# Kernel optimization log

Hardware: AMD Instinct MI355X
Metric: run time of the kernel (lower is better)

The kernel has to match this reference:

```python
import jax, jax.numpy as jnp
import numpy as np

B, N = 4, 512
C_IN, H, W = 1024, 48, 48
IMG_H, IMG_W = 48.0, 48.0
CNN_EMB, BOX_EMB, GCN_OUT = 512, 256, 512
ROWS, COLS = 58, 30
ALPHA = 5.0
K_EDGES = 8 * N  # edges kept per image per graph

# all directed pairs (i != j) of a fully-connected graph on N nodes
_ii, _jj = np.meshgrid(np.arange(N), np.arange(N), indexing='ij')
_m = _ii != _jj
PAIRS = jnp.asarray(np.stack([_ii[_m], _jj[_m]], axis=1).astype(np.int32))  # [E,2]


def setup_inputs():
    key = jax.random.key(0)
    ks = jax.random.split(key, 12)
    x = jax.random.normal(ks[0], (B, C_IN, H, W), jnp.float32)
    # valid boxes (x1<x2, y1<y2) inside the 48x48 feature map
    p = jax.random.uniform(ks[1], (B, N, 2, 2), minval=0.0, maxval=float(W) - 2.0)
    lo = jnp.min(p, axis=2)
    hi = jnp.max(p, axis=2) + 1.0
    boxes = jnp.concatenate([lo, hi], axis=-1)  # [B,N,4] x1,y1,x2,y2

    def lin(k, fi, fo):
        return jax.random.normal(k, (fi, fo), jnp.float32) / np.sqrt(fi)

    return {
        'input': x, 'boxes': boxes,
        'im_scales': jnp.ones((B,), jnp.float32),
        'pdls': jnp.zeros((B,), jnp.float32),
        'pdts': jnp.zeros((B,), jnp.float32),
        'W_dec': jax.random.normal(ks[2], (256, C_IN, 3, 3), jnp.float32) / np.sqrt(C_IN * 9.0),
        'b_dec': jnp.zeros((256,), jnp.float32),
        'W_box': lin(ks[3], 4, BOX_EMB), 'b_box': jnp.zeros((BOX_EMB,), jnp.float32),
        'W_cnn': lin(ks[4], 256 * 4, CNN_EMB), 'b_cnn': jnp.zeros((CNN_EMB,), jnp.float32),
        'W_grow': lin(ks[5], CNN_EMB + BOX_EMB, GCN_OUT), 'b_grow': jnp.zeros((GCN_OUT,), jnp.float32),
        'W_gcol': lin(ks[6], CNN_EMB + BOX_EMB, GCN_OUT), 'b_gcol': jnp.zeros((GCN_OUT,), jnp.float32),
        'W_rcls': lin(ks[7], GCN_OUT, 2 * (ROWS - 1) * 2), 'b_rcls': jnp.zeros((2 * (ROWS - 1) * 2,), jnp.float32),
        'W_ccls': lin(ks[8], GCN_OUT, 2 * (COLS - 1) * 2), 'b_ccls': jnp.zeros((2 * (COLS - 1) * 2,), jnp.float32),
    }


def _bilinear(feat, bidx, py, px):
    # feat [B,C,H,W]; py,px [M,4] sample coords -> [M,4,C]
    Hh, Ww = feat.shape[2], feat.shape[3]
    py = jnp.clip(py, 0.0, Hh - 1.0)
    px = jnp.clip(px, 0.0, Ww - 1.0)
    y0 = jnp.floor(py).astype(jnp.int32)
    x0 = jnp.floor(px).astype(jnp.int32)
    y1 = jnp.minimum(y0 + 1, Hh - 1)
    x1 = jnp.minimum(x0 + 1, Ww - 1)
    wy = (py - y0)[..., None]
    wx = (px - x0)[..., None]
    b = bidx[:, None]
    f00 = feat[b, :, y0, x0]
    f01 = feat[b, :, y0, x1]
    f10 = feat[b, :, y1, x0]
    f11 = feat[b, :, y1, x1]
    return f00 * (1 - wy) * (1 - wx) + f01 * (1 - wy) * wx + f10 * wy * (1 - wx) + f11 * wy * wx


def _roi_align_2x2(feat, boxes, bidx):
    # roi_align output_size=2, spatial_scale=1, one sample per bin (bin center)
    x1, y1, x2, y2 = boxes[:, 0], boxes[:, 1], boxes[:, 2], boxes[:, 3]
    bw = (x2 - x1) / 2.0
    bh = (y2 - y1) / 2.0
    offs = jnp.array([0.5, 1.5], jnp.float32)
    sx = x1[:, None] + offs * bw[:, None]  # [M,2]
    sy = y1[:, None] + offs * bh[:, None]
    py = sy[:, jnp.array([0, 0, 1, 1])]  # (iy, ix) ordering
    px = sx[:, jnp.array([0, 1, 0, 1])]
    val = _bilinear(feat, bidx, py, px)  # [M,4,C]
    return jnp.transpose(val, (0, 2, 1)).reshape(val.shape[0], -1)  # [M, C*2*2]


def _edge_attrs(boxes_i, scale, pdl, pdt):
    org = (boxes_i - jnp.stack([pdl, pdt, pdl, pdt])) / scale
    cx = (org[:, 0] + org[:, 2]) * 0.5
    cy = (org[:, 1] + org[:, 3]) * 0.5
    tb_w = jnp.max(org[:, jnp.array([0, 2])])
    tb_h = jnp.max(org[:, jnp.array([1, 3])])
    s, d = PAIRS[:, 0], PAIRS[:, 1]
    row_attr = jnp.exp(-jnp.square((cy[s] - cy[d]) * ALPHA / tb_h))
    col_attr = jnp.exp(-jnp.square((cx[s] - cx[d]) * ALPHA / tb_w))
    rv, ri = jax.lax.top_k(row_attr, K_EDGES)
    cv, ci = jax.lax.top_k(col_attr, K_EDGES)
    return rv, PAIRS[ri], cv, PAIRS[ci]


def _gcn(x, Wg, bg, edges, ew, num_nodes):
    # PyG GCNConv: self-loops with weight 1, symmetric normalization
    loop = jnp.arange(num_nodes, dtype=edges.dtype)
    src = jnp.concatenate([edges[0], loop])
    dst = jnp.concatenate([edges[1], loop])
    w = jnp.concatenate([ew, jnp.ones((num_nodes,), ew.dtype)])
    deg = jax.ops.segment_sum(w, dst, num_segments=num_nodes)
    dis = jax.lax.rsqrt(deg)  # deg >= 1 thanks to self-loops
    norm = dis[src] * w * dis[dst]
    xw = x @ Wg
    agg = jax.ops.segment_sum(norm[:, None] * xw[src], dst, num_segments=num_nodes)
    return agg + bg


def _forward(input, boxes, im_scales, pdls, pdts, W_dec, b_dec, W_box, b_box,
             W_cnn, b_cnn, W_grow, b_grow, W_gcol, b_gcol, W_rcls, b_rcls, W_ccls, b_ccls):
    Bn = B * N
    flat = boxes.reshape(Bn, 4)
    # box features (relative center / size)
    cx = (flat[:, 0] + flat[:, 2]) / 2.0
    cy = (flat[:, 1] + flat[:, 3]) / 2.0
    bf = jnp.stack([cx / IMG_W, cy / IMG_H,
                    (flat[:, 2] - flat[:, 0]) / IMG_W,
                    (flat[:, 3] - flat[:, 1]) / IMG_H], axis=1)
    box_feat = jax.nn.relu(bf @ W_box + b_box)
    # decode conv + relu
    dec = jax.lax.conv_general_dilated(input, W_dec, (1, 1), 'SAME',
                                       dimension_numbers=('NCHW', 'OIHW', 'NCHW'))
    dec = jax.nn.relu(dec + b_dec[None, :, None, None])
    # roi-align 2x2 + cnn embedding
    bidx = jnp.repeat(jnp.arange(B, dtype=jnp.int32), N)
    cnn = _roi_align_2x2(dec, flat, bidx)
    cnn_feat = jax.nn.relu(cnn @ W_cnn + b_cnn)
    # per-image dense graph -> top-8N row/col edges
    rv, re, cv, ce = jax.vmap(_edge_attrs)(boxes, im_scales, pdls, pdts)
    off = (jnp.arange(B, dtype=jnp.int32) * N)[:, None, None]
    row_edge = (re + off).reshape(-1, 2).T  # [2, B*K]
    col_edge = (ce + off).reshape(-1, 2).T
    row_w = rv.reshape(-1)
    col_w = cv.reshape(-1)
    fusion = jnp.concatenate([box_feat, cnn_feat], axis=1)  # [Bn, 768]
    row_feat = jax.nn.relu(_gcn(fusion, W_grow, b_grow, row_edge, row_w, Bn))
    col_feat = jax.nn.relu(_gcn(fusion, W_gcol, b_gcol, col_edge, col_w, Bn))
    row_score = jax.nn.leaky_relu(row_feat @ W_rcls + b_rcls, 0.01).reshape(Bn, 2, ROWS - 1, 2)
    col_score = jax.nn.leaky_relu(col_feat @ W_ccls + b_ccls, 0.01).reshape(Bn, 2, COLS - 1, 2)
    return row_score, col_score


def reference(input, boxes, im_scales, pdls, pdts, W_dec, b_dec, W_box, b_box,
              W_cnn, b_cnn, W_grow, b_grow, W_gcol, b_gcol, W_rcls, b_rcls, W_ccls, b_ccls):
    return _forward(input, boxes, im_scales, pdls, pdts, W_dec, b_dec, W_box, b_box,
                    W_cnn, b_cnn, W_grow, b_grow, W_gcol, b_gcol,
                    W_rcls, b_rcls, W_ccls, b_ccls)
```

## Files before the change

kernel.cpp:

```cpp
#include <hip/hip_runtime.h>
#include <cstdint>
#include <math.h>

typedef unsigned int u32;
typedef unsigned long long u64;
typedef unsigned short ushort;

typedef __attribute__((ext_vector_type(8))) _Float16 f16x8;
typedef __attribute__((ext_vector_type(4))) _Float16 f16x4;
typedef __attribute__((ext_vector_type(4))) float f32x4;

#define NB    4
#define BnN   2048
#define NE    261632
#define NCHUNK 16
#define ECHUNK 16352
#define KEDGE 4096
#define TIECAP 2048
#define PSLICE 2359296
#define MS    64
#define TS    64

__global__ __launch_bounds__(256) void cvt_x_kernel(
    const float* __restrict__ in, _Float16* __restrict__ xf)
{
    __shared__ _Float16 sh[64][49];
    int cg = blockIdx.x, y = blockIdx.y, b = blockIdx.z;
    int tid = threadIdx.x;
    for (int i = tid; i < 64 * 48; i += 256) {
        int cl = i / 48, x = i - cl * 48;
        sh[cl][x] = (_Float16)in[(((size_t)b * 1024 + cg * 64 + cl) * 48 + y) * 48 + x];
    }
    __syncthreads();
    for (int i = tid; i < 64 * 48; i += 256) {
        int x = i / 64, cl = i - x * 64;
        xf[((size_t)(b * 48 + y) * 48 + x) * 1024 + cg * 64 + cl] = sh[cl][x];
    }
}

__global__ __launch_bounds__(256) void cvt_w_kernel(
    const float* __restrict__ W, _Float16* __restrict__ wf)
{
    __shared__ _Float16 sh[9216];
    int o = blockIdx.x, tid = threadIdx.x;
    for (int g = tid; g < 9216; g += 256)
        sh[g] = (_Float16)W[(size_t)o * 9216 + g];
    __syncthreads();
    for (int g = tid; g < 9216; g += 256) {
        int tap = g >> 10, ch = g & 1023;
        wf[(size_t)o * 9216 + g] = sh[ch * 9 + tap];
    }
}

__global__ __launch_bounds__(256) void cvt_t5_kernel(
    const float* __restrict__ Wc,  _Float16* __restrict__ WcT,
    const float* __restrict__ Wgr, _Float16* __restrict__ WgrT,
    const float* __restrict__ Wgc, _Float16* __restrict__ WgcT,
    const float* __restrict__ Wr,  _Float16* __restrict__ WrT,
    const float* __restrict__ Wcc, _Float16* __restrict__ WccT)
{
    __shared__ _Float16 sh[32][33];
    int bid = blockIdx.x;
    const float* in; _Float16* out; int K, N, tx0, ty0, ntx;
    if (bid < 512)       { in = Wc;  out = WcT;  K = 1024; N = 512; ntx = 16; bid -= 0;    }
    else if (bid < 896)  { in = Wgr; out = WgrT; K = 768;  N = 512; ntx = 16; bid -= 512;  }
    else if (bid < 1280) { in = Wgc; out = WgcT; K = 768;  N = 512; ntx = 16; bid -= 896;  }
    else if (bid < 1408) { in = Wr;  out = WrT;  K = 512;  N = 228; ntx = 8;  bid -= 1280; }
    else                 { in = Wcc; out = WccT; K = 512;  N = 116; ntx = 4;  bid -= 1408; }
    tx0 = (bid % ntx) * 32;
    ty0 = (bid / ntx) * 32;
    int tx = threadIdx.x & 31, ty = threadIdx.x >> 5;
#pragma unroll
    for (int i = 0; i < 4; ++i) {
        int k = ty0 + ty + i * 8, n = tx0 + tx;
        sh[ty + i * 8][tx] = (k < K && n < N) ? (_Float16)in[(size_t)k * N + n] : (_Float16)0.f;
    }
    __syncthreads();
#pragma unroll
    for (int i = 0; i < 4; ++i) {
        int n = tx0 + ty + i * 8, k = ty0 + tx;
        if (n < N && k < K) out[(size_t)n * K + k] = sh[tx][ty + i * 8];
    }
}

#define GLD16(gsrc, ldst)                                                    \
    __builtin_amdgcn_global_load_lds(                                        \
        (const __attribute__((address_space(1))) void*)(gsrc),               \
        (__attribute__((address_space(3))) void*)(ldst), 16, 0, 0)

#define STAGE(cc)                                                            \
    {                                                                        \
        _Pragma("unroll")                                                    \
        for (int it = 0; it < 5; ++it) {                                     \
            if (it * 256 + wv * 64 < 1152)                                   \
                GLD16(wsrc[it] + (cc), &wS[(it * 256 + wv * 64) * 8]);       \
        }                                                                    \
        _Pragma("unroll")                                                    \
        for (int it = 0; it < 8; ++it)                                       \
            GLD16(xsrc[it] + (cc), &xS[(it * 256 + wv * 64) * 8]);           \
    }

__global__ __launch_bounds__(256) void conv_part_kernel(
    const _Float16* __restrict__ xf, const _Float16* __restrict__ wf,
    const _Float16* __restrict__ zbuf, float* __restrict__ pbuf)
{
    __shared__ _Float16 wS[1152 * 8];
    __shared__ _Float16 xS[2048 * 8];
    const int p = blockIdx.x;
    const int L = (p & 7) * 96 + (p >> 3);
    const int og = L & 7;
    const int t  = L >> 3;
    const int xt = t % 6;
    const int bz = t / 6;
    const int y0 = xt * 8;
    const int b  = bz >> 2, ks = bz & 3;
    const int tid = threadIdx.x;
    const int wv = tid >> 6;
    const int ln = tid & 63;
    const int n  = ln & 15;
    const int q  = ln >> 4;

    f32x4 acc[2][2][3];
#pragma unroll
    for (int mt = 0; mt < 2; ++mt)
#pragma unroll
        for (int rr = 0; rr < 2; ++rr)
#pragma unroll
            for (int nt = 0; nt < 3; ++nt) acc[mt][rr][nt] = (f32x4){0.f, 0.f, 0.f, 0.f};

    const _Float16* wsrc[5];
    const _Float16* xsrc[8];
#pragma unroll
    for (int it = 0; it < 5; ++it) {
        int g = it * 256 + tid;
        int gg = (g < 1152) ? g : 0;
        int tap = gg >> 7, r = gg & 127, qq = r >> 5, oc = r & 31;
        wsrc[it] = wf + (size_t)(((og * 32 + oc) * 9 + tap) * 1024 + qq * 8);
    }
#pragma unroll
    for (int it = 0; it < 8; ++it) {
        int g = it * 256 + tid;
        int row = g / 200, r2 = g - row * 200;
        int qq = r2 / 50, c = r2 - qq * 50;
        int gy = y0 + row - 1, gx = c - 1;
        bool inb = (g < 2000) && ((unsigned)gy < 48u) && ((unsigned)gx < 48u);
        xsrc[it] = inb ? (xf + (size_t)(((b * 48 + gy) * 48 + gx) * 1024 + qq * 8)) : zbuf;
    }

    const int c0 = ks * 256;

    STAGE(c0);

#pragma unroll 1
    for (int ci = 0; ci < 8; ++ci) {
        asm volatile("s_waitcnt vmcnt(0)" ::: "memory");
        __syncthreads();

        __builtin_amdgcn_s_setprio(1);
#pragma unroll
        for (int tap = 0; tap < 9; ++tap) {
            const int dy = tap / 3, dx = tap % 3;
            f16x8 a0 = *(const f16x8*)&wS[(tap * 128 + q * 32 + n) * 8];
            f16x8 a1 = *(const f16x8*)&wS[(tap * 128 + q * 32 + 16 + n) * 8];
#pragma unroll
            for (int rr = 0; rr < 2; ++rr) {
                const int row = 2 * wv + rr + dy;
#pragma unroll
                for (int nt = 0; nt < 3; ++nt) {
                    f16x8 bb = *(const f16x8*)&xS[((row * 4 + q) * 50 + nt * 16 + n + dx) * 8];
                    acc[0][rr][nt] = __builtin_amdgcn_mfma_f32_16x16x32_f16(a0, bb, acc[0][rr][nt], 0, 0, 0);
                    acc[1][rr][nt] = __builtin_amdgcn_mfma_f32_16x16x32_f16(a1, bb, acc[1][rr][nt], 0, 0, 0);
                }
            }
        }
        __builtin_amdgcn_s_setprio(0);
        __syncthreads();
        if (ci < 7) STAGE(c0 + (ci + 1) * 32);
    }

#pragma unroll
    for (int rr = 0; rr < 2; ++rr) {
        const int y = y0 + 2 * wv + rr;
#pragma unroll
        for (int mt = 0; mt < 2; ++mt) {
#pragma unroll
            for (int nt = 0; nt < 3; ++nt) {
                int x = nt * 16 + n;
                *(f32x4*)(pbuf + (size_t)ks * PSLICE +
                          ((size_t)(b * 48 + y) * 48 + x) * 256 + og * 32 + mt * 16 + q * 4) = acc[mt][rr][nt];
            }
        }
    }
}

__global__ __launch_bounds__(256) void conv_sum_kernel(
    const float* __restrict__ pbuf, const float* __restrict__ bd,
    _Float16* __restrict__ dec)
{
    size_t idx = (size_t)blockIdx.x * 256 + threadIdx.x;
    size_t e = idx * 4;
    int och = (int)(e & 255);
    f32x4 s0 = *(const f32x4*)(pbuf + e);
    f32x4 s1 = *(const f32x4*)(pbuf + (size_t)PSLICE + e);
    f32x4 s2 = *(const f32x4*)(pbuf + (size_t)2 * PSLICE + e);
    f32x4 s3 = *(const f32x4*)(pbuf + (size_t)3 * PSLICE + e);
    float4 b4 = *(const float4*)(bd + och);
    f16x4 v;
    v.x = (_Float16)fmaxf(s0[0] + s1[0] + s2[0] + s3[0] + b4.x, 0.f);
    v.y = (_Float16)fmaxf(s0[1] + s1[1] + s2[1] + s3[1] + b4.y, 0.f);
    v.z = (_Float16)fmaxf(s0[2] + s1[2] + s2[2] + s3[2] + b4.z, 0.f);
    v.w = (_Float16)fmaxf(s0[3] + s1[3] + s2[3] + s3[3] + b4.w, 0.f);
    *(f16x4*)(dec + e) = v;
}

__global__ __launch_bounds__(256) void roi_box_kernel(
    const _Float16* __restrict__ dec, const float* __restrict__ boxes,
    const float* __restrict__ Wb, const float* __restrict__ bb,
    _Float16* __restrict__ cnn, _Float16* __restrict__ fusion)
{
    int n = blockIdx.x; int c = threadIdx.x;
    int b = n >> 9;
    float x1 = boxes[n * 4 + 0], y1 = boxes[n * 4 + 1];
    float x2 = boxes[n * 4 + 2], y2 = boxes[n * 4 + 3];
    {
        float bf0 = ((x1 + x2) * 0.5f) / 48.f;
        float bf1 = ((y1 + y2) * 0.5f) / 48.f;
        float bf2 = (x2 - x1) / 48.f;
        float bf3 = (y2 - y1) / 48.f;
        float acc = bb[c];
        acc += bf0 * Wb[0 * 256 + c];
        acc += bf1 * Wb[1 * 256 + c];
        acc += bf2 * Wb[2 * 256 + c];
        acc += bf3 * Wb[3 * 256 + c];
        fusion[(size_t)n * 768 + c] = (_Float16)fmaxf(acc, 0.f);
    }
    float bw = (x2 - x1) * 0.5f, bh = (y2 - y1) * 0.5f;
    float sxv[2] = { x1 + 0.5f * bw, x1 + 1.5f * bw };
    float syv[2] = { y1 + 0.5f * bh, y1 + 1.5f * bh };
    float px[4] = { sxv[0], sxv[1], sxv[0], sxv[1] };
    float py[4] = { syv[0], syv[0], syv[1], syv[1] };
    const _Float16* f = dec + (size_t)b * 2304 * 256;
    f16x4 o4;
    float res[4];
#pragma unroll
    for (int p = 0; p < 4; ++p) {
        float yy = fminf(fmaxf(py[p], 0.f), 47.f);
        float xx = fminf(fmaxf(px[p], 0.f), 47.f);
        int y0 = (int)floorf(yy), x0 = (int)floorf(xx);
        int y1i = min(y0 + 1, 47), x1i = min(x0 + 1, 47);
        float wy = yy - (float)y0, wx = xx - (float)x0;
        float f00 = (float)f[(size_t)(y0 * 48 + x0) * 256 + c];
        float f01 = (float)f[(size_t)(y0 * 48 + x1i) * 256 + c];
        float f10 = (float)f[(size_t)(y1i * 48 + x0) * 256 + c];
        float f11 = (float)f[(size_t)(y1i * 48 + x1i) * 256 + c];
        res[p] = f00 * (1.f - wy) * (1.f - wx) + f01 * (1.f - wy) * wx
               + f10 * wy * (1.f - wx) + f11 * wy * wx;
    }
    o4.x = (_Float16)res[0]; o4.y = (_Float16)res[1];
    o4.z = (_Float16)res[2]; o4.w = (_Float16)res[3];
    *(f16x4*)(cnn + (size_t)n * 1024 + c * 4) = o4;
}

template <int ACT, typename OUTT>
__global__ __launch_bounds__(256) void gemm16_kernel(
    const _Float16* __restrict__ A, const _Float16* __restrict__ Bt,
    const float* __restrict__ bias, OUTT* __restrict__ C,
    int M, int N, int K, int ldC)
{
    __shared__ _Float16 aS[64][4][8];
    __shared__ _Float16 bS[64][4][8];
    const int n0 = blockIdx.x * 64, m0 = blockIdx.y * 64;
    const int tid = threadIdx.x;
    const int wv = tid >> 6, ln = tid & 63;
    const int wm = wv & 1, wn = wv >> 1;
    const int lm = ln & 15, lq = ln >> 4;
    const int sr = tid >> 2, sq = tid & 3;

    f32x4 acc[2][2];
#pragma unroll
    for (int i = 0; i < 2; ++i)
#pragma unroll
        for (int j = 0; j < 2; ++j) acc[i][j] = (f32x4){0.f, 0.f, 0.f, 0.f};

    for (int cc = 0; cc < K; cc += 32) {
        *(uint4*)&aS[sr][sq][0] = *(const uint4*)(A + (size_t)(m0 + sr) * K + cc + sq * 8);
        uint4 bv = make_uint4(0u, 0u, 0u, 0u);
        if (n0 + sr < N)
            bv = *(const uint4*)(Bt + (size_t)(n0 + sr) * K + cc + sq * 8);
        *(uint4*)&bS[sr][sq][0] = bv;
        __syncthreads();
        f16x8 af[2], bf[2];
#pragma unroll
        for (int mt = 0; mt < 2; ++mt) af[mt] = *(const f16x8*)&aS[wm * 32 + mt * 16 + lm][lq][0];
#pragma unroll
        for (int nt = 0; nt < 2; ++nt) bf[nt] = *(const f16x8*)&bS[wn * 32 + nt * 16 + lm][lq][0];
#pragma unroll
        for (int mt = 0; mt < 2; ++mt)
#pragma unroll
            for (int nt = 0; nt < 2; ++nt)
                acc[mt][nt] = __builtin_amdgcn_mfma_f32_16x16x32_f16(af[mt], bf[nt], acc[mt][nt], 0, 0, 0);
        __syncthreads();
    }

#pragma unroll
    for (int mt = 0; mt < 2; ++mt) {
#pragma unroll
        for (int nt = 0; nt < 2; ++nt) {
            int col = n0 + wn * 32 + nt * 16 + lm;
            if (col >= N) continue;
            float bs = bias ? bias[col] : 0.f;
#pragma unroll
            for (int r = 0; r < 4; ++r) {
                int row = m0 + wm * 32 + mt * 16 + lq * 4 + r;
                float v = acc[mt][nt][r] + bs;
                if (ACT == 1) v = fmaxf(v, 0.f);
                if (ACT == 2) v = (v >= 0.f) ? v : 0.01f * v;
                C[(size_t)row * ldC + col] = (OUTT)v;
            }
        }
    }
}

__global__ __launch_bounds__(256) void gemm16z_kernel(
    const _Float16* __restrict__ A,
    const _Float16* __restrict__ Bt0, const _Float16* __restrict__ Bt1,
    float* __restrict__ C0, float* __restrict__ C1,
    int M, int N, int K, int ldC)
{
    const _Float16* __restrict__ Bt = blockIdx.z ? Bt1 : Bt0;
    float* __restrict__ C = blockIdx.z ? C1 : C0;
    __shared__ _Float16 aS[64][4][8];
    __shared__ _Float16 bS[64][4][8];
    const int n0 = blockIdx.x * 64, m0 = blockIdx.y * 64;
    const int tid = threadIdx.x;
    const int wv = tid >> 6, ln = tid & 63;
    const int wm = wv & 1, wn = wv >> 1;
    const int lm = ln & 15, lq = ln >> 4;
    const int sr = tid >> 2, sq = tid & 3;

    f32x4 acc[2][2];
#pragma unroll
    for (int i = 0; i < 2; ++i)
#pragma unroll
        for (int j = 0; j < 2; ++j) acc[i][j] = (f32x4){0.f, 0.f, 0.f, 0.f};

    for (int cc = 0; cc < K; cc += 32) {
        *(uint4*)&aS[sr][sq][0] = *(const uint4*)(A + (size_t)(m0 + sr) * K + cc + sq * 8);
        uint4 bv = make_uint4(0u, 0u, 0u, 0u);
        if (n0 + sr < N)
            bv = *(const uint4*)(Bt + (size_t)(n0 + sr) * K + cc + sq * 8);
        *(uint4*)&bS[sr][sq][0] = bv;
        __syncthreads();
        f16x8 af[2], bf[2];
#pragma unroll
        for (int mt = 0; mt < 2; ++mt) af[mt] = *(const f16x8*)&aS[wm * 32 + mt * 16 + lm][lq][0];
#pragma unroll
        for (int nt = 0; nt < 2; ++nt) bf[nt] = *(const f16x8*)&bS[wn * 32 + nt * 16 + lm][lq][0];
#pragma unroll
        for (int mt = 0; mt < 2; ++mt)
#pragma unroll
            for (int nt = 0; nt < 2; ++nt)
                acc[mt][nt] = __builtin_amdgcn_mfma_f32_16x16x32_f16(af[mt], bf[nt], acc[mt][nt], 0, 0, 0);
        __syncthreads();
    }

#pragma unroll
    for (int mt = 0; mt < 2; ++mt) {
#pragma unroll
        for (int nt = 0; nt < 2; ++nt) {
            int col = n0 + wn * 32 + nt * 16 + lm;
            if (col >= N) continue;
#pragma unroll
            for (int r = 0; r < 4; ++r) {
                int row = m0 + wm * 32 + mt * 16 + lq * 4 + r;
                C[(size_t)row * ldC + col] = acc[mt][nt][r];
            }
        }
    }
}

__device__ __forceinline__ float compute_sv_tb(
    const float* __restrict__ boxes, const float* __restrict__ scales,
    const float* __restrict__ pdls, const float* __restrict__ pdts,
    int b, int t, float* sv, float* red)
{
    int tid = threadIdx.x;
    float pdl = pdls[b], pdt = pdts[b], sc = scales[b];
    if (tid < 512) {
        const float* bx = boxes + (size_t)(b * 512 + tid) * 4;
        float o0 = (bx[0] - pdl) / sc;
        float o1 = (bx[1] - pdt) / sc;
        float o2 = (bx[2] - pdl) / sc;
        float o3 = (bx[3] - pdt) / sc;
        sv[tid]  = (t == 0) ? (o1 + o3) * 0.5f : (o0 + o2) * 0.5f;
        red[tid] = (t == 0) ? fmaxf(o1, o3)    : fmaxf(o0, o2);
    }
    __syncthreads();
    for (int s = 256; s > 0; s >>= 1) {
        if (tid < s) red[tid] = fmaxf(red[tid], red[tid + s]);
        __syncthreads();
    }
    float tbv = red[0];
    __syncthreads();
    return tbv;
}

#define QBITS(e, QB)                                                   \
    {                                                                  \
        int i_ = (e) / 511; int jj_ = (e) - i_ * 511;                  \
        int j_ = jj_ + (jj_ >= i_ ? 1 : 0);                            \
        float diff_ = sv[i_] - sv[j_];                                 \
        float u_ = (diff_ * 5.0f) / tbv;                               \
        float q_ = u_ * u_;                                            \
        QB = __float_as_uint(q_);                                      \
    }

__global__ __launch_bounds__(1024) void histA_kernel(
    const float* __restrict__ boxes, const float* __restrict__ scales,
    const float* __restrict__ pdls, const float* __restrict__ pdts,
    u32* __restrict__ gpart)
{
    __shared__ float sv[512]; __shared__ float red[512];
    __shared__ u32 lh[4096];
    const int sel = blockIdx.y, b = sel >> 1, t = sel & 1;
    const int tid = threadIdx.x;
    for (int i = tid; i < 4096; i += 1024) lh[i] = 0;
    const float tbv = compute_sv_tb(boxes, scales, pdls, pdts, b, t, sv, red);
    const int e1 = min((int)(blockIdx.x + 1) * ECHUNK, NE);
    for (int e = blockIdx.x * ECHUNK + tid; e < e1; e += 1024) {
        u32 qb; QBITS(e, qb);
        atomicAdd(&lh[qb >> 20], 1u);
    }
    __syncthreads();
    u32* G = gpart + ((size_t)sel * NCHUNK + blockIdx.x) * 4096;
    for (int i = tid; i < 4096; i += 1024) G[i] = lh[i];
}

__global__ __launch_bounds__(1024) void scanA_kernel(
    const u32* __restrict__ gpart, u32* __restrict__ meta)
{
    const int sel = blockIdx.x, tid = threadIdx.x;
    __shared__ u32 bins[4096];
    __shared__ u32 sc[2][1024];
    for (int b = tid; b < 4096; b += 1024) {
        u32 s = 0;
        for (int c = 0; c < NCHUNK; ++c) s += gpart[((size_t)sel * NCHUNK + c) * 4096 + b];
        bins[b] = s;
    }
    __syncthreads();
    u32 part = 0;
#pragma unroll
    for (int j = 0; j < 4; ++j) part += bins[tid * 4 + j];
    sc[0][tid] = part;
    __syncthreads();
    int src = 0;
    for (int st = 1; st < 1024; st <<= 1) {
        sc[1 - src][tid] = sc[src][tid] + (tid >= st ? sc[src][tid - st] : 0);
        __syncthreads(); src = 1 - src;
    }
    u32 inc = sc[src][tid], exc = inc - part;
    if (exc < (u32)KEDGE && (u32)KEDGE <= inc) {
        u32 cum = exc;
        for (int j = 0; j < 4; ++j) {
            u32 c = bins[tid * 4 + j];
            if (cum + c >= (u32)KEDGE) {
                meta[sel * MS + 0] = (u32)(tid * 4 + j);
                meta[sel * MS + 1] = (u32)KEDGE - cum;
                break;
            }
            cum += c;
        }
    }
}

__global__ __launch_bounds__(1024) void histB_kernel(
    const float* __restrict__ boxes, const float* __restrict__ scales,
    const float* __restrict__ pdls, const float* __restrict__ pdts,
    const u32* __restrict__ meta, u32* __restrict__ gpart)
{
    __shared__ float sv[512]; __shared__ float red[512];
    __shared__ u32 lh[4096];
    const int sel = blockIdx.y, b = sel >> 1, t = sel & 1;
    const int tid = threadIdx.x;
    for (int i = tid; i < 4096; i += 1024) lh[i] = 0;
    const float tbv = compute_sv_tb(boxes, scales, pdls, pdts, b, t, sv, red);
    const u32 p12 = meta[sel * MS + 0];
    const int e1 = min((int)(blockIdx.x + 1) * ECHUNK, NE);
    for (int e = blockIdx.x * ECHUNK + tid; e < e1; e += 1024) {
        u32 qb; QBITS(e, qb);
        if ((qb >> 20) == p12) atomicAdd(&lh[(qb >> 8) & 0xFFF], 1u);
    }
    __syncthreads();
    u32* G = gpart + ((size_t)sel * NCHUNK + blockIdx.x) * 4096;
    for (int i = tid; i < 4096; i += 1024) G[i] = lh[i];
}

__global__ __launch_bounds__(1024) void scanB_kernel(
    const u32* __restrict__ gpart, u32* __restrict__ meta)
{
    const int sel = blockIdx.x, tid = threadIdx.x;
    const u32 TH = meta[sel * MS + 1];
    __shared__ u32 bins[4096];
    __shared__ u32 sc[2][1024];
    for (int b = tid; b < 4096; b += 1024) {
        u32 s = 0;
        for (int c = 0; c < NCHUNK; ++c) s += gpart[((size_t)sel * NCHUNK + c) * 4096 + b];
        bins[b] = s;
    }
    __syncthreads();
    u32 part = 0;
#pragma unroll
    for (int j = 0; j < 4; ++j) part += bins[tid * 4 + j];
    sc[0][tid] = part;
    __syncthreads();
    int src = 0;
    for (int st = 1; st < 1024; st <<= 1) {
        sc[1 - src][tid] = sc[src][tid] + (tid >= st ? sc[src][tid - st] : 0);
        __syncthreads(); src = 1 - src;
    }
    u32 inc = sc[src][tid], exc = inc - part;
    if (exc < TH && TH <= inc) {
        u32 cum = exc;
        for (int j = 0; j < 4; ++j) {
            u32 c = bins[tid * 4 + j];
            if (cum + c >= TH) {
                meta[sel * MS + 6] = (meta[sel * MS + 0] << 12) | (u32)(tid * 4 + j);
                meta[sel * MS + 7] = TH - cum;
                break;
            }
            cum += c;
        }
    }
}

__global__ __launch_bounds__(1024) void histC_kernel(
    const float* __restrict__ boxes, const float* __restrict__ scales,
    const float* __restrict__ pdls, const float* __restrict__ pdts,
    const u32* __restrict__ meta, u32* __restrict__ gpart)
{
    __shared__ float sv[512]; __shared__ float red[512];
    __shared__ u32 lh[256];
    const int sel = blockIdx.y, b = sel >> 1, t = sel & 1;
    const int tid = threadIdx.x;
    if (tid < 256) lh[tid] = 0;
    const float tbv = compute_sv_tb(boxes, scales, pdls, pdts, b, t, sv, red);
    const u32 p24 = meta[sel * MS + 6];
    const int e1 = min((int)(blockIdx.x + 1) * ECHUNK, NE);
    for (int e = blockIdx.x * ECHUNK + tid; e < e1; e += 1024) {
        u32 qb; QBITS(e, qb);
        if ((qb >> 8) == p24) atomicAdd(&lh[qb & 0xFF], 1u);
    }
    __syncthreads();
    u32* G = gpart + ((size_t)sel * NCHUNK + blockIdx.x) * 256;
    if (tid < 256) G[tid] = lh[tid];
}

__global__ __launch_bounds__(256) void scanC_kernel(
    const u32* __restrict__ gpart, u32* __restrict__ meta)
{
    const int sel = blockIdx.x, tid = threadIdx.x;
    const u32 TH = meta[sel * MS + 7];
    __shared__ u32 bins[256];
    __shared__ u32 sc[2][256];
    __shared__ u32 s_qstar;
    u32 s = 0;
    for (int c = 0; c < NCHUNK; ++c) s += gpart[((size_t)sel * NCHUNK + c) * 256 + tid];
    bins[tid] = s;
    sc[0][tid] = s;
    __syncthreads();
    int src = 0;
    for (int st = 1; st < 256; st <<= 1) {
        sc[1 - src][tid] = sc[src][tid] + (tid >= st ? sc[src][tid - st] : 0);
        __syncthreads(); src = 1 - src;
    }
    u32 inc = sc[src][tid], exc = inc - bins[tid];
    if (exc < TH && TH <= inc)
        s_qstar = (meta[sel * MS + 6] << 8) | (u32)tid;
    __syncthreads();
    if (tid == 0) {
        u32 prefix = s_qstar;
        float qstar = __uint_as_float(prefix);
        float wstar = (float)exp(-(double)qstar);
        u32 lo = 0, hi = prefix;
        while (lo < hi) {
            u32 mid = (lo + hi) >> 1;
            float wm = (float)exp(-(double)__uint_as_float(mid));
            if (wm > wstar) lo = mid + 1; else hi = mid;
        }
        meta[sel * MS + 2] = lo;
        lo = prefix; hi = 0x7F800000u;
        while (lo < hi) {
            u32 mid = (lo + hi + 1) >> 1;
            float wm = (float)exp(-(double)__uint_as_float(mid));
            if (wm < wstar) hi = mid - 1; else lo = mid;
        }
        meta[sel * MS + 3] = lo;
        meta[sel * MS + 4] = __float_as_uint(wstar);
    }
}

__global__ __launch_bounds__(1024) void emit_kernel(
    const float* __restrict__ boxes, const float* __restrict__ scales,
    const float* __restrict__ pdls, const float* __restrict__ pdts,
    u32* __restrict__ meta, int* __restrict__ tiebuf, int* __restrict__ tiecnt,
    int* __restrict__ es, int* __restrict__ ed, float* __restrict__ ewt,
    int* __restrict__ indeg, float* __restrict__ degw)
{
    __shared__ float sv[512]; __shared__ float red[512];
    __shared__ int s_wcnt, s_tcnt, s_wbase, s_tbase;
    const int sel = blockIdx.y, b = sel >> 1, t = sel & 1;
    const int tid = threadIdx.x;
    const float tbv = compute_sv_tb(boxes, scales, pdls, pdts, b, t, sv, red);
    const u32 qlo = meta[sel * MS + 2], qhi = meta[sel * MS + 3];
    const int base = t * 16384 + b * 4096;
    const int e0 = blockIdx.x * ECHUNK + tid;
    const int e1 = min((int)(blockIdx.x + 1) * ECHUNK, NE);
    if (tid == 0) { s_wcnt = 0; s_tcnt = 0; }
    __syncthreads();
    int myw = 0, myt = 0;
    for (int e = e0; e < e1; e += 1024) {
        u32 qb; QBITS(e, qb);
        if (qb < qlo) ++myw;
        else if (qb <= qhi) ++myt;
    }
    if (myw) atomicAdd(&s_wcnt, myw);
    if (myt) atomicAdd(&s_tcnt, myt);
    __syncthreads();
    if (tid == 0) {
        s_wbase = (s_wcnt > 0) ? (int)atomicAdd(&meta[sel * MS + 5], (u32)s_wcnt) : 0;
        s_tbase = (s_tcnt > 0) ? atomicAdd(&tiecnt[sel * TS], s_tcnt) : 0;
        s_wcnt = 0; s_tcnt = 0;
    }
    __syncthreads();
    for (int e = e0; e < e1; e += 1024) {
        u32 qb; QBITS(e, qb);
        if (qb < qlo) {
            int i = e / 511; int jj = e - i * 511; int j = jj + (jj >= i ? 1 : 0);
            float wval = (float)exp(-(double)__uint_as_float(qb));
            int slot = s_wbase + atomicAdd(&s_wcnt, 1);
            es[base + slot] = b * 512 + i;
            ed[base + slot] = b * 512 + j;
            ewt[base + slot] = wval;
            atomicAdd(&indeg[t * 2048 + b * 512 + j], 1);
            atomicAdd(&degw[t * 2048 + b * 512 + j], wval);
        } else if (qb <= qhi) {
            int p = s_tbase + atomicAdd(&s_tcnt, 1);
            if (p < TIECAP) tiebuf[sel * TIECAP + p] = e;
        }
    }
}

__global__ __launch_bounds__(1024) void tie_scan_fill_kernel(
    u32* __restrict__ meta, const int* __restrict__ tiebuf, const int* __restrict__ tiecnt,
    int* __restrict__ es, int* __restrict__ ed, float* __restrict__ ewt,
    int* __restrict__ indeg, float* __restrict__ degw,
    int* __restrict__ offs, float* __restrict__ dis, int* __restrict__ csr)
{
    __shared__ int bufA[2048], bufB[2048];
    __shared__ int fill_l[2048];
    const int t = blockIdx.x, tid = threadIdx.x;
    for (int b = 0; b < 4; ++b) {
        int sel = b * 2 + t;
        int m = min(tiecnt[sel * TS], TIECAP);
        int r = KEDGE - (int)meta[sel * MS + 5];
        float wt = __uint_as_float(meta[sel * MS + 4]);
        int base = t * 16384 + b * 4096;
        for (int k = tid; k < m; k += 1024) {
            int e = tiebuf[sel * TIECAP + k];
            int rank = 0;
            for (int l = 0; l < m; ++l) rank += (tiebuf[sel * TIECAP + l] < e) ? 1 : 0;
            if (rank < r) {
                int i = e / 511; int jj = e - i * 511; int j = jj + (jj >= i ? 1 : 0);
                int slot = (int)atomicAdd(&meta[sel * MS + 5], 1u);
                es[base + slot] = b * 512 + i;
                ed[base + slot] = b * 512 + j;
                ewt[base + slot] = wt;
                atomicAdd(&indeg[t * 2048 + b * 512 + j], 1);
                atomicAdd(&degw[t * 2048 + b * 512 + j], wt);
            }
        }
    }
    __threadfence();
    __syncthreads();
    bufA[tid] = indeg[t * 2048 + tid];
    bufA[tid + 1024] = indeg[t * 2048 + tid + 1024];
    fill_l[tid] = 0; fill_l[tid + 1024] = 0;
    __syncthreads();
    int* src = bufA; int* dst = bufB;
    for (int st = 1; st < 2048; st <<= 1) {
        dst[tid] = src[tid] + (tid >= st ? src[tid - st] : 0);
        int k1 = tid + 1024;
        dst[k1] = src[k1] + (k1 >= st ? src[k1 - st] : 0);
        __syncthreads();
        int* tmp = src; src = dst; dst = tmp;
    }
    int off0 = (tid == 0) ? 0 : src[tid - 1];
    int off1 = src[tid + 1023];
    __syncthreads();
    dst[tid] = off0; dst[tid + 1024] = off1;
    offs[t * 2048 + tid] = off0;
    offs[t * 2048 + tid + 1024] = off1;
    dis[t * 2048 + tid] = 1.0f / sqrtf(1.0f + degw[t * 2048 + tid]);
    dis[t * 2048 + tid + 1024] = 1.0f / sqrtf(1.0f + degw[t * 2048 + tid + 1024]);
    __syncthreads();
    for (int e = tid; e < 16384; e += 1024) {
        int dl = ed[t * 16384 + e] & 2047;
        int pos = dst[dl] + atomicAdd(&fill_l[dl], 1);
        csr[t * 16384 + pos] = e;
    }
}

__global__ __launch_bounds__(256) void gcn_agg_kernel(
    const float* __restrict__ xw_row, const float* __restrict__ xw_col,
    const float* __restrict__ b_row, const float* __restrict__ b_col,
    const int* __restrict__ es, const float* __restrict__ ew,
    const int* __restrict__ csr, const int* __restrict__ offs,
    const int* __restrict__ indeg, const float* __restrict__ dis,
    _Float16* __restrict__ feat_row, _Float16* __restrict__ feat_col)
{
    int d = blockIdx.x; int t = blockIdx.y;
    const float* xw = t ? xw_col : xw_row;
    const float* bg = t ? b_col : b_row;
    _Float16* out = t ? feat_col : feat_row;
    int f0 = threadIdx.x, f1 = threadIdx.x + 256;
    float dd = dis[t * 2048 + d];
    float a0 = dd * dd * xw[(size_t)d * 512 + f0];
    float a1 = dd * dd * xw[(size_t)d * 512 + f1];
    int st = offs[t * 2048 + d], cnt = indeg[t * 2048 + d];
    for (int k = 0; k < cnt; ++k) {
        int e = csr[t * 16384 + st + k];
        int s = es[t * 16384 + e];
        float w = ew[t * 16384 + e];
        float coef = dis[t * 2048 + s] * w * dd;
        a0 += coef * xw[(size_t)s * 512 + f0];
        a1 += coef * xw[(size_t)s * 512 + f1];
    }
    a0 += bg[f0]; a1 += bg[f1];
    out[(size_t)d * 512 + f0] = (_Float16)fmaxf(a0, 0.f);
    out[(size_t)d * 512 + f1] = (_Float16)fmaxf(a1, 0.f);
}

extern "C" void kernel_launch(void* const* d_in, const int* in_sizes, int n_in,
                              void* d_out, int out_size, void* d_ws, size_t ws_size,
                              hipStream_t stream)
{
    const float* x      = (const float*)d_in[0];
    const float* boxes  = (const float*)d_in[1];
    const float* scales = (const float*)d_in[2];
    const float* pdls   = (const float*)d_in[3];
    const float* pdts   = (const float*)d_in[4];
    const float* W_dec  = (const float*)d_in[5];
    const float* b_dec  = (const float*)d_in[6];
    const float* W_box  = (const float*)d_in[7];
    const float* b_box  = (const float*)d_in[8];
    const float* W_cnn  = (const float*)d_in[9];
    const float* b_cnn  = (const float*)d_in[10];
    const float* W_grow = (const float*)d_in[11];
    const float* b_grow = (const float*)d_in[12];
    const float* W_gcol = (const float*)d_in[13];
    const float* b_gcol = (const float*)d_in[14];
    const float* W_rcls = (const float*)d_in[15];
    const float* b_rcls = (const float*)d_in[16];
    const float* W_ccls = (const float*)d_in[17];
    const float* b_ccls = (const float*)d_in[18];

    char* ws = (char*)d_ws;
    size_t off = 0;
    auto alloc = [&](size_t bytes) -> void* {
        void* p = ws + off;
        off = (off + bytes + 255) & ~(size_t)255;
        return p;
    };
    _Float16* xf16   = (_Float16*)alloc((size_t)4 * 2304 * 1024 * 2);
    _Float16* wf16   = (_Float16*)alloc((size_t)256 * 9216 * 2);
    _Float16* dec    = (_Float16*)alloc((size_t)4 * 2304 * 256 * 2);
    float*    pbuf   = (float*)   alloc((size_t)4 * PSLICE * 4);
    _Float16* cnn    = (_Float16*)alloc((size_t)2048 * 1024 * 2);
    _Float16* fusion = (_Float16*)alloc((size_t)2048 * 768 * 2);
    _Float16* WcT    = (_Float16*)alloc((size_t)512 * 1024 * 2);
    _Float16* WgrT   = (_Float16*)alloc((size_t)512 * 768 * 2);
    _Float16* WgcT   = (_Float16*)alloc((size_t)512 * 768 * 2);
    _Float16* WrT    = (_Float16*)alloc((size_t)228 * 512 * 2);
    _Float16* WccT   = (_Float16*)alloc((size_t)116 * 512 * 2);
    float* xw        = (float*)alloc((size_t)2097152 * 4);
    _Float16* feats  = (_Float16*)alloc((size_t)2 * 2048 * 512 * 2);
    int*  es     = (int*)  alloc((size_t)2 * 16384 * 4);
    int*  ed     = (int*)  alloc((size_t)2 * 16384 * 4);
    float* ewt   = (float*)alloc((size_t)2 * 16384 * 4);
    int*  offsA  = (int*)  alloc((size_t)4096 * 4);
    float* dis   = (float*)alloc((size_t)4096 * 4);
    int*  csr    = (int*)  alloc((size_t)2 * 16384 * 4);
    int*  tiebuf = (int*)  alloc((size_t)8 * TIECAP * 4);
    u32*  gpartA = (u32*)  alloc((size_t)8 * NCHUNK * 4096 * 4);
    u32*  gpartB = (u32*)  alloc((size_t)8 * NCHUNK * 4096 * 4);
    u32*  gpartC = (u32*)  alloc((size_t)8 * NCHUNK * 256 * 4);
    size_t z0 = off;
    u32*  meta   = (u32*)  alloc((size_t)8 * MS * 4);
    int*  tiecnt = (int*)  alloc((size_t)8 * TS * 4);
    int*  indeg  = (int*)  alloc((size_t)4096 * 4);
    float* degw  = (float*)alloc((size_t)4096 * 4);
    _Float16* zbuf = (_Float16*)alloc((size_t)4096);
    size_t z1 = off;

    float* out = (float*)d_out;

    hipMemsetAsync(ws + z0, 0, z1 - z0, stream);

    cvt_x_kernel<<<dim3(16, 48, 4), 256, 0, stream>>>(x, xf16);
    cvt_w_kernel<<<256, 256, 0, stream>>>(W_dec, wf16);
    conv_part_kernel<<<dim3(768), 256, 0, stream>>>(xf16, wf16, zbuf, pbuf);
    conv_sum_kernel<<<2304, 256, 0, stream>>>(pbuf, b_dec, dec);
    roi_box_kernel<<<2048, 256, 0, stream>>>(dec, boxes, W_box, b_box, cnn, fusion);
    cvt_t5_kernel<<<1472, 256, 0, stream>>>(W_cnn, WcT, W_grow, WgrT, W_gcol, WgcT,
                                            W_rcls, WrT, W_ccls, WccT);
    gemm16_kernel<1, _Float16><<<dim3(8, 32), 256, 0, stream>>>(cnn, WcT, b_cnn, fusion + 256, 2048, 512, 1024, 768);
    histA_kernel<<<dim3(NCHUNK, 8), 1024, 0, stream>>>(boxes, scales, pdls, pdts, gpartA);
    scanA_kernel<<<8, 1024, 0, stream>>>(gpartA, meta);
    histB_kernel<<<dim3(NCHUNK, 8), 1024, 0, stream>>>(boxes, scales, pdls, pdts, meta, gpartB);
    scanB_kernel<<<8, 1024, 0, stream>>>(gpartB, meta);
    histC_kernel<<<dim3(NCHUNK, 8), 1024, 0, stream>>>(boxes, scales, pdls, pdts, meta, gpartC);
    scanC_kernel<<<8, 256, 0, stream>>>(gpartC, meta);
    emit_kernel<<<dim3(NCHUNK, 8), 1024, 0, stream>>>(boxes, scales, pdls, pdts, meta,
                                                      tiebuf, tiecnt, es, ed, ewt, indeg, degw);
    tie_scan_fill_kernel<<<2, 1024, 0, stream>>>(meta, tiebuf, tiecnt, es, ed, ewt,
                                                 indeg, degw, offsA, dis, csr);
    gemm16z_kernel<<<dim3(8, 32, 2), 256, 0, stream>>>(fusion, WgrT, WgcT, xw, xw + 1048576,
                                                       2048, 512, 768, 512);
    gcn_agg_kernel<<<dim3(2048, 2), 256, 0, stream>>>(xw, xw + 1048576, b_grow, b_gcol,
                                                      es, ewt, csr, offsA, indeg, dis,
                                                      feats, feats + (size_t)2048 * 512);
    gemm16_kernel<2, float><<<dim3(4, 32), 256, 0, stream>>>(feats, WrT, b_rcls, out, 2048, 228, 512, 228);
    gemm16_kernel<2, float><<<dim3(2, 32), 256, 0, stream>>>(feats + (size_t)2048 * 512, WccT, b_ccls,
                                                             out + (size_t)2048 * 228, 2048, 116, 512, 116);
}
```

Measured before the change: 362.7 us.

## Double-buffer GEMM tiles via direct-to-LDS loads and reuse conv input rows across taps

The small GEMM kernels now stage A/B tiles with global_load_lds into double-buffered shared memory. The next K-slice is prefetched while the current one is multiplied, replacing the register round-trip and the two full syncthreads per step. The conv inner loop is restructured so each input row's nine B fragments are loaded once into registers and reused across the dy taps via rotating buffers. It also adds a launch_bounds occupancy hint of 3. The trade-offs are more register pressure in the conv kernel, a dummy zero buffer for out-of-range B rows, and reliance on hand-placed vmcnt waits for correctness.

```diff
diff --git a/kernel.cpp b/kernel.cpp
--- a/kernel.cpp
+++ b/kernel.cpp
@@ -20,6 +20,11 @@
 #define PSLICE 2359296
 #define MS    64
 #define TS    64
+
+#define GLD16(gsrc, ldst)                                                    \
+    __builtin_amdgcn_global_load_lds(                                        \
+        (const __attribute__((address_space(1))) void*)(gsrc),               \
+        (__attribute__((address_space(3))) void*)(ldst), 16, 0, 0)
 
 __global__ __launch_bounds__(256) void cvt_x_kernel(
     const float* __restrict__ in, _Float16* __restrict__ xf)
@@ -83,11 +88,6 @@
     }
 }
 
-#define GLD16(gsrc, ldst)                                                    \
-    __builtin_amdgcn_global_load_lds(                                        \
-        (const __attribute__((address_space(1))) void*)(gsrc),               \
-        (__attribute__((address_space(3))) void*)(ldst), 16, 0, 0)
-
 #define STAGE(cc)                                                            \
     {                                                                        \
         _Pragma("unroll")                                                    \
@@ -100,7 +100,34 @@
             GLD16(xsrc[it] + (cc), &xS[(it * 256 + wv * 64) * 8]);           \
     }
 
-__global__ __launch_bounds__(256) void conv_part_kernel(
+#define LDB(BUF, R)                                                          \
+    {                                                                        \
+        _Pragma("unroll")                                                    \
+        for (int u = 0; u < 9; ++u) {                                        \
+            int nt_ = u / 3, dx_ = u % 3;                                    \
+            BUF[u] = *(const f16x8*)&xS[(((R) * 4 + q) * 50 + nt_ * 16 + n + dx_) * 8]; \
+        }                                                                    \
+    }
+
+#define DOTAP(TAP, BLO, BHI)                                                 \
+    {                                                                        \
+        _Pragma("unroll")                                                    \
+        for (int dx_ = 0; dx_ < 3; ++dx_) {                                  \
+            f16x8 a0 = *(const f16x8*)&wS[(((TAP) + dx_) * 128 + q * 32 + n) * 8];      \
+            f16x8 a1 = *(const f16x8*)&wS[(((TAP) + dx_) * 128 + q * 32 + 16 + n) * 8]; \
+            _Pragma("unroll")                                                \
+            for (int nt_ = 0; nt_ < 3; ++nt_) {                              \
+                f16x8 blo = BLO[nt_ * 3 + dx_];                              \
+                f16x8 bhi = BHI[nt_ * 3 + dx_];                              \
+                acc[0][0][nt_] = __builtin_amdgcn_mfma_f32_16x16x32_f16(a0, blo, acc[0][0][nt_], 0, 0, 0); \
+                acc[1][0][nt_] = __builtin_amdgcn_mfma_f32_16x16x32_f16(a1, blo, acc[1][0][nt_], 0, 0, 0); \
+                acc[0][1][nt_] = __builtin_amdgcn_mfma_f32_16x16x32_f16(a0, bhi, acc[0][1][nt_], 0, 0, 0); \
+                acc[1][1][nt_] = __builtin_amdgcn_mfma_f32_16x16x32_f16(a1, bhi, acc[1][1][nt_], 0, 0, 0); \
+            }                                                                \
+        }                                                                    \
+    }
+
+__global__ __launch_bounds__(256, 3) void conv_part_kernel(
     const _Float16* __restrict__ xf, const _Float16* __restrict__ wf,
     const _Float16* __restrict__ zbuf, float* __restrict__ pbuf)
 {
@@ -148,6 +175,7 @@
     }
 
     const int c0 = ks * 256;
+    const int rbase = 2 * wv;
 
     STAGE(c0);
 
@@ -157,22 +185,14 @@
         __syncthreads();
 
         __builtin_amdgcn_s_setprio(1);
-#pragma unroll
-        for (int tap = 0; tap < 9; ++tap) {
-            const int dy = tap / 3, dx = tap % 3;
-            f16x8 a0 = *(const f16x8*)&wS[(tap * 128 + q * 32 + n) * 8];
-            f16x8 a1 = *(const f16x8*)&wS[(tap * 128 + q * 32 + 16 + n) * 8];
-#pragma unroll
-            for (int rr = 0; rr < 2; ++rr) {
-                const int row = 2 * wv + rr + dy;
-#pragma unroll
-                for (int nt = 0; nt < 3; ++nt) {
-                    f16x8 bb = *(const f16x8*)&xS[((row * 4 + q) * 50 + nt * 16 + n + dx) * 8];
-                    acc[0][rr][nt] = __builtin_amdgcn_mfma_f32_16x16x32_f16(a0, bb, acc[0][rr][nt], 0, 0, 0);
-                    acc[1][rr][nt] = __builtin_amdgcn_mfma_f32_16x16x32_f16(a1, bb, acc[1][rr][nt], 0, 0, 0);
-                }
-            }
-        }
+        f16x8 bA[9], bB[9];
+        LDB(bA, rbase + 0);
+        LDB(bB, rbase + 1);
+        DOTAP(0, bA, bB);
+        LDB(bA, rbase + 2);
+        DOTAP(3, bB, bA);
+        LDB(bB, rbase + 3);
+        DOTAP(6, bA, bB);
         __builtin_amdgcn_s_setprio(0);
         __syncthreads();
         if (ci < 7) STAGE(c0 + (ci + 1) * 32);
@@ -261,14 +281,21 @@
     *(f16x4*)(cnn + (size_t)n * 1024 + c * 4) = o4;
 }
 
+#define GEMM_STAGE(cc, bi)                                                   \
+    {                                                                        \
+        GLD16(asrc + (cc), &aS[bi][(wv * 64) * 8]);                          \
+        GLD16(bsrc + (cc), &bS[bi][(wv * 64) * 8]);                          \
+    }
+
 template <int ACT, typename OUTT>
 __global__ __launch_bounds__(256) void gemm16_kernel(
     const _Float16* __restrict__ A, const _Float16* __restrict__ Bt,
+    const _Float16* __restrict__ zbuf,
     const float* __restrict__ bias, OUTT* __restrict__ C,
     int M, int N, int K, int ldC)
 {
-    __shared__ _Float16 aS[64][4][8];
-    __shared__ _Float16 bS[64][4][8];
+    __shared__ _Float16 aS[2][256 * 8];
+    __shared__ _Float16 bS[2][256 * 8];
     const int n0 = blockIdx.x * 64, m0 = blockIdx.y * 64;
     const int tid = threadIdx.x;
     const int wv = tid >> 6, ln = tid & 63;
@@ -276,30 +303,39 @@
     const int lm = ln & 15, lq = ln >> 4;
     const int sr = tid >> 2, sq = tid & 3;
 
+    const _Float16* asrc = A + (size_t)(m0 + sr) * K + sq * 8;
+    const _Float16* bsrc = (n0 + sr < N) ? (Bt + (size_t)(n0 + sr) * K + sq * 8) : zbuf;
+
     f32x4 acc[2][2];
 #pragma unroll
     for (int i = 0; i < 2; ++i)
 #pragma unroll
         for (int j = 0; j < 2; ++j) acc[i][j] = (f32x4){0.f, 0.f, 0.f, 0.f};
 
-    for (int cc = 0; cc < K; cc += 32) {
-        *(uint4*)&aS[sr][sq][0] = *(const uint4*)(A + (size_t)(m0 + sr) * K + cc + sq * 8);
-        uint4 bv = make_uint4(0u, 0u, 0u, 0u);
-        if (n0 + sr < N)
-            bv = *(const uint4*)(Bt + (size_t)(n0 + sr) * K + cc + sq * 8);
-        *(uint4*)&bS[sr][sq][0] = bv;
-        __syncthreads();
+    const int NT = K >> 5;
+    GEMM_STAGE(0, 0);
+#pragma unroll 1
+    for (int it = 0; it < NT; ++it) {
+        const int bi = it & 1;
+        if (it + 1 < NT) {
+            GEMM_STAGE((it + 1) * 32, bi ^ 1);
+            asm volatile("s_waitcnt vmcnt(2)" ::: "memory");
+        } else {
+            asm volatile("s_waitcnt vmcnt(0)" ::: "memory");
+        }
+        __builtin_amdgcn_s_barrier();
         f16x8 af[2], bf[2];
 #pragma unroll
-        for (int mt = 0; mt < 2; ++mt) af[mt] = *(const f16x8*)&aS[wm * 32 + mt * 16 + lm][lq][0];
-#pragma unroll
-        for (int nt = 0; nt < 2; ++nt) bf[nt] = *(const f16x8*)&bS[wn * 32 + nt * 16 + lm][lq][0];
+        for (int mt = 0; mt < 2; ++mt) af[mt] = *(const f16x8*)&aS[bi][(wm * 32 + mt * 16 + lm) * 32 + lq * 8];
+#pragma unroll
+        for (int nt = 0; nt < 2; ++nt) bf[nt] = *(const f16x8*)&bS[bi][(wn * 32 + nt * 16 + lm) * 32 + lq * 8];
 #pragma unroll
         for (int mt = 0; mt < 2; ++mt)
 #pragma unroll
             for (int nt = 0; nt < 2; ++nt)
                 acc[mt][nt] = __builtin_amdgcn_mfma_f32_16x16x32_f16(af[mt], bf[nt], acc[mt][nt], 0, 0, 0);
-        __syncthreads();
+        __builtin_amdgcn_sched_barrier(0);
+        __builtin_amdgcn_s_barrier();
     }
 
 #pragma unroll
@@ -324,13 +360,14 @@
 __global__ __launch_bounds__(256) void gemm16z_kernel(
     const _Float16* __restrict__ A,
     const _Float16* __restrict__ Bt0, const _Float16* __restrict__ Bt1,
+    const _Float16* __restrict__ zbuf,
     float* __restrict__ C0, float* __restrict__ C1,
     int M, int N, int K, int ldC)
 {
     const _Float16* __restrict__ Bt = blockIdx.z ? Bt1 : Bt0;
     float* __restrict__ C = blockIdx.z ? C1 : C0;
-    __shared__ _Float16 aS[64][4][8];
-    __shared__ _Float16 bS[64][4][8];
+    __shared__ _Float16 aS[2][256 * 8];
+    __shared__ _Float16 bS[2][256 * 8];
     const int n0 = blockIdx.x * 64, m0 = blockIdx.y * 64;
     const int tid = threadIdx.x;
     const int wv = tid >> 6, ln = tid & 63;
@@ -338,30 +375,39 @@
     const int lm = ln & 15, lq = ln >> 4;
     const int sr = tid >> 2, sq = tid & 3;
 
+    const _Float16* asrc = A + (size_t)(m0 + sr) * K + sq * 8;
+    const _Float16* bsrc = (n0 + sr < N) ? (Bt + (size_t)(n0 + sr) * K + sq * 8) : zbuf;
+
     f32x4 acc[2][2];
 #pragma unroll
     for (int i = 0; i < 2; ++i)
 #pragma unroll
         for (int j = 0; j < 2; ++j) acc[i][j] = (f32x4){0.f, 0.f, 0.f, 0.f};
 
-    for (int cc = 0; cc < K; cc += 32) {
-        *(uint4*)&aS[sr][sq][0] = *(const uint4*)(A + (size_t)(m0 + sr) * K + cc + sq * 8);
-        uint4 bv = make_uint4(0u, 0u, 0u, 0u);
-        if (n0 + sr < N)
-            bv = *(const uint4*)(Bt + (size_t)(n0 + sr) * K + cc + sq * 8);
-        *(uint4*)&bS[sr][sq][0] = bv;
-        __syncthreads();
+    const int NT = K >> 5;
+    GEMM_STAGE(0, 0);
+#pragma unroll 1
+    for (int it = 0; it < NT; ++it) {
+        const int bi = it & 1;
+        if (it + 1 < NT) {
+            GEMM_STAGE((it + 1) * 32, bi ^ 1);
+            asm volatile("s_waitcnt vmcnt(2)" ::: "memory");
+        } else {
+            asm volatile("s_waitcnt vmcnt(0)" ::: "memory");
+        }
+        __builtin_amdgcn_s_barrier();
         f16x8 af[2], bf[2];
 #pragma unroll
-        for (int mt = 0; mt < 2; ++mt) af[mt] = *(const f16x8*)&aS[wm * 32 + mt * 16 + lm][lq][0];
-#pragma unroll
-        for (int nt = 0; nt < 2; ++nt) bf[nt] = *(const f16x8*)&bS[wn * 32 + nt * 16 + lm][lq][0];
+        for (int mt = 0; mt < 2; ++mt) af[mt] = *(const f16x8*)&aS[bi][(wm * 32 + mt * 16 + lm) * 32 + lq * 8];
+#pragma unroll
+        for (int nt = 0; nt < 2; ++nt) bf[nt] = *(const f16x8*)&bS[bi][(wn * 32 + nt * 16 + lm) * 32 + lq * 8];
 #pragma unroll
         for (int mt = 0; mt < 2; ++mt)
 #pragma unroll
             for (int nt = 0; nt < 2; ++nt)
                 acc[mt][nt] = __builtin_amdgcn_mfma_f32_16x16x32_f16(af[mt], bf[nt], acc[mt][nt], 0, 0, 0);
-        __syncthreads();
+        __builtin_amdgcn_sched_barrier(0);
+        __builtin_amdgcn_s_barrier();
     }
 
 #pragma unroll
@@ -813,7 +859,7 @@
     roi_box_kernel<<<2048, 256, 0, stream>>>(dec, boxes, W_box, b_box, cnn, fusion);
     cvt_t5_kernel<<<1472, 256, 0, stream>>>(W_cnn, WcT, W_grow, WgrT, W_gcol, WgcT,
                                             W_rcls, WrT, W_ccls, WccT);
-    gemm16_kernel<1, _Float16><<<dim3(8, 32), 256, 0, stream>>>(cnn, WcT, b_cnn, fusion + 256, 2048, 512, 1024, 768);
+    gemm16_kernel<1, _Float16><<<dim3(8, 32), 256, 0, stream>>>(cnn, WcT, zbuf, b_cnn, fusion + 256, 2048, 512, 1024, 768);
     histA_kernel<<<dim3(NCHUNK, 8), 1024, 0, stream>>>(boxes, scales, pdls, pdts, gpartA);
     scanA_kernel<<<8, 1024, 0, stream>>>(gpartA, meta);
     histB_kernel<<<dim3(NCHUNK, 8), 1024, 0, stream>>>(boxes, scales, pdls, pdts, meta, gpartB);
@@ -824,12 +870,12 @@
                                                       tiebuf, tiecnt, es, ed, ewt, indeg, degw);
     tie_scan_fill_kernel<<<2, 1024, 0, stream>>>(meta, tiebuf, tiecnt, es, ed, ewt,
                                                  indeg, degw, offsA, dis, csr);
-    gemm16z_kernel<<<dim3(8, 32, 2), 256, 0, stream>>>(fusion, WgrT, WgcT, xw, xw + 1048576,
+    gemm16z_kernel<<<dim3(8, 32, 2), 256, 0, stream>>>(fusion, WgrT, WgcT, zbuf, xw, xw + 1048576,
                                                        2048, 512, 768, 512);
     gcn_agg_kernel<<<dim3(2048, 2), 256, 0, stream>>>(xw, xw + 1048576, b_grow, b_gcol,
                                                       es, ewt, csr, offsA, indeg, dis,
                                                       feats, feats + (size_t)2048 * 512);
-    gemm16_kernel<2, float><<<dim3(4, 32), 256, 0, stream>>>(feats, WrT, b_rcls, out, 2048, 228, 512, 228);
-    gemm16_kernel<2, float><<<dim3(2, 32), 256, 0, stream>>>(feats + (size_t)2048 * 512, WccT, b_ccls,
+    gemm16_kernel<2, float><<<dim3(4, 32), 256, 0, stream>>>(feats, WrT, zbuf, b_rcls, out, 2048, 228, 512, 228);
+    gemm16_kernel<2, float><<<dim3(2, 32), 256, 0, stream>>>(feats + (size_t)2048 * 512, WccT, zbuf, b_ccls,
                                                              out + (size_t)2048 * 228, 2048, 116, 512, 116);
 }
```

Result: faster. 348.2 us (-4.0%).
